# Kernel optimization log

Hardware: AMD Instinct MI355X
Metric: run time of the kernel (lower is better)

The kernel has to match this reference:

```python
import jax, jax.numpy as jnp
import numpy as np

MARGIN = 0.3
HARD_FACTOR = 0.0
EPS = 1e-6


def setup_inputs() -> dict:
    key = jax.random.key(0)
    k1, k2 = jax.random.split(key)
    inputs = jax.random.normal(k1, (4096, 256), dtype=jnp.float32)
    targets = jax.random.randint(k2, (4096,), 0, 512, dtype=jnp.int64)
    return {"inputs": inputs, "targets": targets}


def reference(inputs, targets):
    n = inputs.shape[0]
    half = n // 2
    # L2-normalize features (matches normalize(): x / (||x|| + 1e-6))
    x = inputs / (jnp.linalg.norm(inputs, axis=-1, keepdims=True) + EPS)
    # pairwise euclidean distances, clamped at 1e-6 before sqrt
    sq = jnp.sum(x * x, axis=1)                      # (n,)
    dist = sq[:, None] + sq[None, :] - 2.0 * (x @ x.T)  # (n, n)
    dist = jnp.sqrt(jnp.clip(dist, EPS))
    # same-identity mask
    mask = targets[:, None] == targets[None, :]      # (n, n) bool
    # rows in the first half mine over columns [half:n], rows in the
    # second half mine over columns [0:half] -> gather the opposite half
    first = (jnp.arange(n) < half)[:, None]          # (n, 1)
    d_o = jnp.where(first, dist[:, half:], dist[:, :half])  # (n, half)
    m_o = jnp.where(first, mask[:, half:], mask[:, :half])  # (n, half) bool
    pos_any = jnp.any(m_o, axis=1)
    neg_any = jnp.any(~m_o, axis=1)
    dist_ap = jnp.where(pos_any,
                        jnp.max(jnp.where(m_o, d_o, -jnp.inf), axis=1),
                        0.0)
    dist_an = jnp.where(neg_any,
                        jnp.min(jnp.where(m_o, jnp.inf, d_o), axis=1),
                        1.0)
    dist_ap = dist_ap * (1.0 + HARD_FACTOR)
    dist_an = dist_an * (1.0 - HARD_FACTOR)
    # MarginRankingLoss(margin)(dist_an, dist_ap, y=1) =
    #   mean(relu(-(dist_an - dist_ap) + margin))
    loss = jnp.mean(jax.nn.relu(dist_ap - dist_an + MARGIN))
    return loss
```

## Files before the change

kernel.cpp:

```cpp
#include <hip/hip_runtime.h>
#include <math.h>

#define N 4096
#define D 256
#define HALF 2048
#define MARGIN 0.3f

#define BM 64
#define NTB (HALF/BM)

typedef __attribute__((ext_vector_type(8))) short bf16x8;
typedef __attribute__((ext_vector_type(4))) float f32x4;

__device__ __forceinline__ unsigned short bf16_rne(float x) {
    unsigned int u = __float_as_uint(x);
    return (unsigned short)((u + 0x7fffu + ((u >> 16) & 1u)) >> 16);
}

__device__ __forceinline__ void load_lds16(const unsigned short* g,
                                           unsigned short* l) {
    __builtin_amdgcn_global_load_lds(
        (const __attribute__((address_space(1))) void*)g,
        (__attribute__((address_space(3))) void*)l, 16, 0, 0);
}

__global__ __launch_bounds__(256) void k_norm(const float* __restrict__ in,
                                              unsigned short* __restrict__ xnb,
                                              float* __restrict__ sq) {
    const int wave = threadIdx.x >> 6, lane = threadIdx.x & 63;
    const int row = blockIdx.x * 4 + wave;
    float4 v = *(const float4*)&in[(size_t)row * D + lane * 4];
    float s = v.x * v.x + v.y * v.y + v.z * v.z + v.w * v.w;
#pragma unroll
    for (int o = 1; o < 64; o <<= 1) s += __shfl_xor(s, o, 64);
    float nrm = sqrtf(s);
    float inv = 1.0f / (nrm + 1e-6f);
    ushort4 h;
    h.x = bf16_rne(v.x * inv);
    h.y = bf16_rne(v.y * inv);
    h.z = bf16_rne(v.z * inv);
    h.w = bf16_rne(v.w * inv);
    *(ushort4*)&xnb[(size_t)row * D + lane * 4] = h;
    if (lane == 0) {
        float q = nrm * inv;
        sq[row] = q * q;
    }
}

__global__ __launch_bounds__(256) void k_tile(const unsigned short* __restrict__ xnb,
                                              const float* __restrict__ sq,
                                              const int* __restrict__ tg,
                                              float* __restrict__ rowap,
                                              float* __restrict__ rowan,
                                              float* __restrict__ colap,
                                              float* __restrict__ colan) {
    __shared__ unsigned short As[BM * D];
    __shared__ unsigned short Bs[BM * D];
    __shared__ int sra[BM], srn[BM], sca[BM], scn[BM];

    const int bi = blockIdx.y, bj = blockIdx.x;
    const int I0 = bi * BM;
    const int J0 = bj * BM;
    const int tid = threadIdx.x;
    const int wave = tid >> 6, lane = tid & 63;
    const int wm = wave >> 1, wn = wave & 1;
    const int lrow = lane & 15, lquad = lane >> 4;

    {
        const int slot = lane & 31;
        const int rsub = lane >> 5;
        const int swz = (wave * 2 + rsub) & 7;
        const int goff = ((slot ^ swz) << 3);
#pragma unroll
        for (int i = 0; i < 8; ++i) {
            int r0 = i * 8 + wave * 2;
            int rl = r0 + rsub;
            load_lds16(&xnb[(size_t)(I0 + rl) * D + goff], &As[r0 * D]);
            load_lds16(&xnb[(size_t)(HALF + J0 + rl) * D + goff], &Bs[r0 * D]);
        }
    }
    __syncthreads();

    f32x4 acc[2][2];
#pragma unroll
    for (int a = 0; a < 2; ++a)
#pragma unroll
        for (int b = 0; b < 2; ++b) acc[a][b] = (f32x4){0.f, 0.f, 0.f, 0.f};

    const int rsw = lrow & 7;
#pragma unroll
    for (int k0 = 0; k0 < D; k0 += 32) {
        const int c0 = (k0 >> 3) + lquad;
        const int co = ((c0 ^ rsw) << 3);
        bf16x8 af[2], bfr[2];
#pragma unroll
        for (int mi = 0; mi < 2; ++mi)
            af[mi] = *(const bf16x8*)&As[(wm * 32 + mi * 16 + lrow) * D + co];
#pragma unroll
        for (int nj = 0; nj < 2; ++nj)
            bfr[nj] = *(const bf16x8*)&Bs[(wn * 32 + nj * 16 + lrow) * D + co];
#pragma unroll
        for (int mi = 0; mi < 2; ++mi)
#pragma unroll
            for (int nj = 0; nj < 2; ++nj)
                acc[mi][nj] = __builtin_amdgcn_mfma_f32_16x16x32_bf16(
                    af[mi], bfr[nj], acc[mi][nj], 0, 0, 0);
    }

    float sqi[2][4], sqj[2];
    int tgi[2][4], tgj[2];
#pragma unroll
    for (int mi = 0; mi < 2; ++mi)
#pragma unroll
        for (int r = 0; r < 4; ++r) {
            int lr = wm * 32 + mi * 16 + lquad * 4 + r;
            sqi[mi][r] = sq[I0 + lr];
            tgi[mi][r] = tg[I0 + lr];
        }
#pragma unroll
    for (int nj = 0; nj < 2; ++nj) {
        int lc = wn * 32 + nj * 16 + lrow;
        sqj[nj] = sq[HALF + J0 + lc];
        tgj[nj] = tg[HALF + J0 + lc];
    }

    const float INF = __int_as_float(0x7f800000);
    float rap[2][4], ran[2][4], capv[2], canv[2];
#pragma unroll
    for (int mi = 0; mi < 2; ++mi)
#pragma unroll
        for (int r = 0; r < 4; ++r) { rap[mi][r] = 0.f; ran[mi][r] = INF; }
#pragma unroll
    for (int nj = 0; nj < 2; ++nj) { capv[nj] = 0.f; canv[nj] = INF; }

#pragma unroll
    for (int mi = 0; mi < 2; ++mi)
#pragma unroll
        for (int nj = 0; nj < 2; ++nj)
#pragma unroll
            for (int r = 0; r < 4; ++r) {
                float d2 = sqi[mi][r] + sqj[nj] - 2.0f * acc[mi][nj][r];
                float d = sqrtf(fmaxf(d2, 1e-6f));
                if (tgi[mi][r] == tgj[nj]) {
                    rap[mi][r] = fmaxf(rap[mi][r], d);
                    capv[nj] = fmaxf(capv[nj], d);
                } else {
                    ran[mi][r] = fminf(ran[mi][r], d);
                    canv[nj] = fminf(canv[nj], d);
                }
            }

#pragma unroll
    for (int mi = 0; mi < 2; ++mi)
#pragma unroll
        for (int r = 0; r < 4; ++r)
#pragma unroll
            for (int o = 1; o < 16; o <<= 1) {
                rap[mi][r] = fmaxf(rap[mi][r], __shfl_xor(rap[mi][r], o, 64));
                ran[mi][r] = fminf(ran[mi][r], __shfl_xor(ran[mi][r], o, 64));
            }
#pragma unroll
    for (int nj = 0; nj < 2; ++nj)
#pragma unroll
        for (int o = 16; o < 64; o <<= 1) {
            capv[nj] = fmaxf(capv[nj], __shfl_xor(capv[nj], o, 64));
            canv[nj] = fminf(canv[nj], __shfl_xor(canv[nj], o, 64));
        }

    if (tid < BM) { sra[tid] = 0; srn[tid] = 0x7f800000;
                    sca[tid] = 0; scn[tid] = 0x7f800000; }
    __syncthreads();
    if (lrow == 0) {
#pragma unroll
        for (int mi = 0; mi < 2; ++mi)
#pragma unroll
            for (int r = 0; r < 4; ++r) {
                int lr = wm * 32 + mi * 16 + lquad * 4 + r;
                atomicMax(&sra[lr], __float_as_int(rap[mi][r]));
                atomicMin(&srn[lr], __float_as_int(ran[mi][r]));
            }
    }
    if (lquad == 0) {
#pragma unroll
        for (int nj = 0; nj < 2; ++nj) {
            int lc = wn * 32 + nj * 16 + lrow;
            atomicMax(&sca[lc], __float_as_int(capv[nj]));
            atomicMin(&scn[lc], __float_as_int(canv[nj]));
        }
    }
    __syncthreads();
    if (tid < BM) {
        rowap[bj * HALF + I0 + tid] = __int_as_float(sra[tid]);
        rowan[bj * HALF + I0 + tid] = __int_as_float(srn[tid]);
        colap[bi * HALF + J0 + tid] = __int_as_float(sca[tid]);
        colan[bi * HALF + J0 + tid] = __int_as_float(scn[tid]);
    }
}

__global__ __launch_bounds__(256) void k_reduce(const float* __restrict__ rowap,
                                                const float* __restrict__ rowan,
                                                const float* __restrict__ colap,
                                                const float* __restrict__ colan,
                                                float* __restrict__ bsum) {
    const int t = threadIdx.x;
    const int gid = blockIdx.x * 256 + t;
    const float INF = __int_as_float(0x7f800000);
    float ap = 0.f, an = INF;
    if (gid < HALF) {
#pragma unroll
        for (int b = 0; b < NTB; ++b) {
            ap = fmaxf(ap, rowap[b * HALF + gid]);
            an = fminf(an, rowan[b * HALF + gid]);
        }
    } else {
        int j = gid - HALF;
#pragma unroll
        for (int b = 0; b < NTB; ++b) {
            ap = fmaxf(ap, colap[b * HALF + j]);
            an = fminf(an, colan[b * HALF + j]);
        }
    }
    if (an == INF) an = 1.0f;
    float v = ap - an + MARGIN;
    float s = (v > 0.f) ? v : 0.f;
#pragma unroll
    for (int o = 32; o > 0; o >>= 1) s += __shfl_down(s, o, 64);
    __shared__ float wsum[4];
    if ((t & 63) == 0) wsum[t >> 6] = s;
    __syncthreads();
    if (t == 0) bsum[blockIdx.x] = wsum[0] + wsum[1] + wsum[2] + wsum[3];
}

__global__ void k_final(const float* __restrict__ bsum, float* __restrict__ out) {
    if (threadIdx.x == 0) {
        float tot = 0.f;
#pragma unroll
        for (int b = 0; b < 16; ++b) tot += bsum[b];
        out[0] = tot / (float)N;
    }
}

extern "C" void kernel_launch(void* const* d_in, const int* in_sizes, int n_in,
                              void* d_out, int out_size, void* d_ws, size_t ws_size,
                              hipStream_t stream) {
    const float* in = (const float*)d_in[0];
    const int* tg = (const int*)d_in[1];
    float* out = (float*)d_out;

    unsigned short* xnb = (unsigned short*)d_ws;
    float* sq = (float*)(xnb + (size_t)N * D);
    float* rowap = sq + N;
    float* rowan = rowap + NTB * HALF;
    float* colap = rowan + NTB * HALF;
    float* colan = colap + NTB * HALF;
    float* bsum  = colan + NTB * HALF;

    k_norm<<<N / 4, 256, 0, stream>>>(in, xnb, sq);
    k_tile<<<dim3(NTB, NTB), 256, 0, stream>>>(xnb, sq, tg,
                                               rowap, rowan, colap, colan);
    k_reduce<<<16, 256, 0, stream>>>(rowap, rowan, colap, colan, bsum);
    k_final<<<1, 64, 0, stream>>>(bsum, out);
}
```

Measured before the change: 83.39 us.

## Pad LDS tiles, use register-staged loads, fuse final reduction via atomics

```diff
diff --git a/kernel.cpp b/kernel.cpp
--- a/kernel.cpp
+++ b/kernel.cpp
@@ -8,6 +8,7 @@
 
 #define BM 64
 #define NTB (HALF/BM)
+#define LDA 264
 
 typedef __attribute__((ext_vector_type(8))) short bf16x8;
 typedef __attribute__((ext_vector_type(4))) float f32x4;
@@ -17,16 +18,11 @@
     return (unsigned short)((u + 0x7fffu + ((u >> 16) & 1u)) >> 16);
 }
 
-__device__ __forceinline__ void load_lds16(const unsigned short* g,
-                                           unsigned short* l) {
-    __builtin_amdgcn_global_load_lds(
-        (const __attribute__((address_space(1))) void*)g,
-        (__attribute__((address_space(3))) void*)l, 16, 0, 0);
-}
-
 __global__ __launch_bounds__(256) void k_norm(const float* __restrict__ in,
                                               unsigned short* __restrict__ xnb,
-                                              float* __restrict__ sq) {
+                                              float* __restrict__ sq,
+                                              float* __restrict__ acc_sum,
+                                              int* __restrict__ acc_cnt) {
     const int wave = threadIdx.x >> 6, lane = threadIdx.x & 63;
     const int row = blockIdx.x * 4 + wave;
     float4 v = *(const float4*)&in[(size_t)row * D + lane * 4];
@@ -45,6 +41,10 @@
         float q = nrm * inv;
         sq[row] = q * q;
     }
+    if (blockIdx.x == 0 && threadIdx.x == 0) {
+        *acc_sum = 0.f;
+        *acc_cnt = 0;
+    }
 }
 
 __global__ __launch_bounds__(256) void k_tile(const unsigned short* __restrict__ xnb,
@@ -54,8 +54,8 @@
                                               float* __restrict__ rowan,
                                               float* __restrict__ colap,
                                               float* __restrict__ colan) {
-    __shared__ unsigned short As[BM * D];
-    __shared__ unsigned short Bs[BM * D];
+    __shared__ unsigned short As[BM * LDA];
+    __shared__ unsigned short Bs[BM * LDA];
     __shared__ int sra[BM], srn[BM], sca[BM], scn[BM];
 
     const int bi = blockIdx.y, bj = blockIdx.x;
@@ -67,16 +67,22 @@
     const int lrow = lane & 15, lquad = lane >> 4;
 
     {
-        const int slot = lane & 31;
-        const int rsub = lane >> 5;
-        const int swz = (wave * 2 + rsub) & 7;
-        const int goff = ((slot ^ swz) << 3);
+        const int chunk = tid & 31;
+        const int rp = tid >> 5;
+        const unsigned short* Agp = xnb + (size_t)I0 * D;
+        const unsigned short* Bgp = xnb + (size_t)(HALF + J0) * D;
+        uint4 av[8], bv[8];
 #pragma unroll
         for (int i = 0; i < 8; ++i) {
-            int r0 = i * 8 + wave * 2;
-            int rl = r0 + rsub;
-            load_lds16(&xnb[(size_t)(I0 + rl) * D + goff], &As[r0 * D]);
-            load_lds16(&xnb[(size_t)(HALF + J0 + rl) * D + goff], &Bs[r0 * D]);
+            int r = i * 8 + rp;
+            av[i] = *(const uint4*)&Agp[(size_t)r * D + chunk * 8];
+            bv[i] = *(const uint4*)&Bgp[(size_t)r * D + chunk * 8];
+        }
+#pragma unroll
+        for (int i = 0; i < 8; ++i) {
+            int r = i * 8 + rp;
+            *(uint4*)&As[r * LDA + chunk * 8] = av[i];
+            *(uint4*)&Bs[r * LDA + chunk * 8] = bv[i];
         }
     }
     __syncthreads();
@@ -87,18 +93,15 @@
 #pragma unroll
         for (int b = 0; b < 2; ++b) acc[a][b] = (f32x4){0.f, 0.f, 0.f, 0.f};
 
-    const int rsw = lrow & 7;
 #pragma unroll
     for (int k0 = 0; k0 < D; k0 += 32) {
-        const int c0 = (k0 >> 3) + lquad;
-        const int co = ((c0 ^ rsw) << 3);
         bf16x8 af[2], bfr[2];
 #pragma unroll
         for (int mi = 0; mi < 2; ++mi)
-            af[mi] = *(const bf16x8*)&As[(wm * 32 + mi * 16 + lrow) * D + co];
+            af[mi] = *(const bf16x8*)&As[(wm * 32 + mi * 16 + lrow) * LDA + k0 + lquad * 8];
 #pragma unroll
         for (int nj = 0; nj < 2; ++nj)
-            bfr[nj] = *(const bf16x8*)&Bs[(wn * 32 + nj * 16 + lrow) * D + co];
+            bfr[nj] = *(const bf16x8*)&Bs[(wn * 32 + nj * 16 + lrow) * LDA + k0 + lquad * 8];
 #pragma unroll
         for (int mi = 0; mi < 2; ++mi)
 #pragma unroll
@@ -197,13 +200,15 @@
     }
 }
 
-__global__ __launch_bounds__(256) void k_reduce(const float* __restrict__ rowap,
-                                                const float* __restrict__ rowan,
-                                                const float* __restrict__ colap,
-                                                const float* __restrict__ colan,
-                                                float* __restrict__ bsum) {
-    const int t = threadIdx.x;
-    const int gid = blockIdx.x * 256 + t;
+__global__ __launch_bounds__(64) void k_reduce(const float* __restrict__ rowap,
+                                               const float* __restrict__ rowan,
+                                               const float* __restrict__ colap,
+                                               const float* __restrict__ colan,
+                                               float* __restrict__ acc_sum,
+                                               int* __restrict__ acc_cnt,
+                                               float* __restrict__ out) {
+    const int lane = threadIdx.x;
+    const int gid = blockIdx.x * 64 + lane;
     const float INF = __int_as_float(0x7f800000);
     float ap = 0.f, an = INF;
     if (gid < HALF) {
@@ -224,19 +229,15 @@
     float v = ap - an + MARGIN;
     float s = (v > 0.f) ? v : 0.f;
 #pragma unroll
-    for (int o = 32; o > 0; o >>= 1) s += __shfl_down(s, o, 64);
-    __shared__ float wsum[4];
-    if ((t & 63) == 0) wsum[t >> 6] = s;
-    __syncthreads();
-    if (t == 0) bsum[blockIdx.x] = wsum[0] + wsum[1] + wsum[2] + wsum[3];
-}
-
-__global__ void k_final(const float* __restrict__ bsum, float* __restrict__ out) {
-    if (threadIdx.x == 0) {
-        float tot = 0.f;
-#pragma unroll
-        for (int b = 0; b < 16; ++b) tot += bsum[b];
-        out[0] = tot / (float)N;
+    for (int o = 1; o < 64; o <<= 1) s += __shfl_xor(s, o, 64);
+    if (lane == 0) {
+        atomicAdd(acc_sum, s);
+        __threadfence();
+        int old = atomicAdd(acc_cnt, 1);
+        if (old == 63) {
+            float tot = atomicAdd(acc_sum, 0.0f);
+            out[0] = tot / (float)N;
+        }
     }
 }
 
@@ -253,11 +254,12 @@
     float* rowan = rowap + NTB * HALF;
     float* colap = rowan + NTB * HALF;
     float* colan = colap + NTB * HALF;
-    float* bsum  = colan + NTB * HALF;
-
-    k_norm<<<N / 4, 256, 0, stream>>>(in, xnb, sq);
+    float* acc_sum = colan + NTB * HALF;
+    int* acc_cnt = (int*)(acc_sum + 1);
+
+    k_norm<<<N / 4, 256, 0, stream>>>(in, xnb, sq, acc_sum, acc_cnt);
     k_tile<<<dim3(NTB, NTB), 256, 0, stream>>>(xnb, sq, tg,
                                                rowap, rowan, colap, colan);
-    k_reduce<<<16, 256, 0, stream>>>(rowap, rowan, colap, colan, bsum);
-    k_final<<<1, 64, 0, stream>>>(bsum, out);
-}
+    k_reduce<<<64, 64, 0, stream>>>(rowap, rowan, colap, colan,
+                                    acc_sum, acc_cnt, out);
+}
```

New measurement: 82.44 us. Within noise of the previous version (-1.1%).
